# Kernel optimization log

Measured on AMD Instinct MI355X. Metric: run time of the kernel, lower is better.

Reference implementation:

```python
import jax, jax.numpy as jnp
import numpy as np

S, C1, C2, N = 4096, 2048, 2048, 1024


def setup_inputs() -> dict:
    key = jax.random.key(0)
    k1, k2, k3, k4 = jax.random.split(key, 4)
    # child log-likelihoods (samples, child_nodes); modest scale so exp() stays finite,
    # matching the (numerically naive) torch forward which exps without max-subtraction.
    ll1 = jax.random.normal(k1, (S, C1), dtype=jnp.float32)
    ll2 = jax.random.normal(k2, (S, C2), dtype=jnp.float32)
    # log edge weights, one tensor per child layer: (nodes, child_nodes)
    w1 = jax.random.normal(k3, (N, C1), dtype=jnp.float32)
    w2 = jax.random.normal(k4, (N, C2), dtype=jnp.float32)
    return {"ll1": ll1, "ll2": ll2, "w1": w1, "w2": w2}


def reference(ll1, ll2, w1, w2):
    # Per child layer: sum_c exp(ll[s,c] + w[n,c]) == exp(ll) @ exp(w).T  -> (S, N)
    # (same math as unsqueeze/repeat/exp/sum in the torch code, without the (S,C,N) blowup)
    result = jnp.exp(ll1) @ jnp.exp(w1).T + jnp.exp(ll2) @ jnp.exp(w2).T  # (S, N)
    # per-node log normalization constant over concatenated weights
    log_z = jax.nn.logsumexp(jnp.concatenate([w1, w2], axis=1), axis=1)  # (N,)
    return jnp.log(result) - log_z[None, :]
```

## Files before the change

### kernel.cpp

```cpp
#include <hip/hip_runtime.h>

#define S_DIM 4096
#define C_DIM 2048
#define N_DIM 1024
#define K_DIM 4096

#define BM 128
#define BN 128
#define BK 32
#define NT (K_DIM / BK)
#define TILE_BYTES 16384
#define NBUF 8

typedef __attribute__((ext_vector_type(8))) short bf16x8;
typedef __attribute__((ext_vector_type(4))) float f32x4;

__device__ static inline unsigned short f2bf(float f) {
    unsigned int u = __float_as_uint(f);
    u += 0x7FFFu + ((u >> 16) & 1u);
    return (unsigned short)(u >> 16);
}

__global__ void exp_ll_kernel(const float* __restrict__ ll1,
                              const float* __restrict__ ll2,
                              unsigned short* __restrict__ A) {
    const int total4 = S_DIM * C_DIM / 4;
    int stride = gridDim.x * blockDim.x;
    for (int i = blockIdx.x * blockDim.x + threadIdx.x; i < total4; i += stride) {
        int e = i << 2;
        int r = e >> 11;
        int c = e & 2047;
        size_t dst = ((size_t)r << 12) + c;
        float4 v = *reinterpret_cast<const float4*>(ll1 + e);
        ushort4 o;
        o.x = f2bf(__expf(v.x)); o.y = f2bf(__expf(v.y));
        o.z = f2bf(__expf(v.z)); o.w = f2bf(__expf(v.w));
        *reinterpret_cast<ushort4*>(A + dst) = o;
        float4 u = *reinterpret_cast<const float4*>(ll2 + e);
        ushort4 p;
        p.x = f2bf(__expf(u.x)); p.y = f2bf(__expf(u.y));
        p.z = f2bf(__expf(u.z)); p.w = f2bf(__expf(u.w));
        *reinterpret_cast<ushort4*>(A + dst + C_DIM) = p;
    }
}

__global__ void w_kernel(const float* __restrict__ w1,
                         const float* __restrict__ w2,
                         unsigned short* __restrict__ B,
                         float* __restrict__ lz) {
    const int n = blockIdx.x;
    const int tid = threadIdx.x;
    const int lane = tid & 63, wv = tid >> 6;
    const float* r1 = w1 + ((size_t)n << 11);
    const float* r2 = w2 + ((size_t)n << 11);
    float4 v0 = *reinterpret_cast<const float4*>(r1 + tid * 8);
    float4 v1 = *reinterpret_cast<const float4*>(r1 + tid * 8 + 4);
    float4 u0 = *reinterpret_cast<const float4*>(r2 + tid * 8);
    float4 u1 = *reinterpret_cast<const float4*>(r2 + tid * 8 + 4);

    float mx = fmaxf(fmaxf(fmaxf(v0.x, v0.y), fmaxf(v0.z, v0.w)),
                     fmaxf(fmaxf(v1.x, v1.y), fmaxf(v1.z, v1.w)));
    mx = fmaxf(mx, fmaxf(fmaxf(fmaxf(u0.x, u0.y), fmaxf(u0.z, u0.w)),
                          fmaxf(fmaxf(u1.x, u1.y), fmaxf(u1.z, u1.w))));
    #pragma unroll
    for (int off = 32; off > 0; off >>= 1) mx = fmaxf(mx, __shfl_xor(mx, off));
    __shared__ float red[4];
    if (lane == 0) red[wv] = mx;
    __syncthreads();
    mx = fmaxf(fmaxf(red[0], red[1]), fmaxf(red[2], red[3]));

    float s = __expf(v0.x - mx) + __expf(v0.y - mx) + __expf(v0.z - mx) + __expf(v0.w - mx)
            + __expf(v1.x - mx) + __expf(v1.y - mx) + __expf(v1.z - mx) + __expf(v1.w - mx)
            + __expf(u0.x - mx) + __expf(u0.y - mx) + __expf(u0.z - mx) + __expf(u0.w - mx)
            + __expf(u1.x - mx) + __expf(u1.y - mx) + __expf(u1.z - mx) + __expf(u1.w - mx);
    #pragma unroll
    for (int off = 32; off > 0; off >>= 1) s += __shfl_xor(s, off);
    __shared__ float red2[4];
    if (lane == 0) red2[wv] = s;
    __syncthreads();
    if (tid == 0)
        lz[n] = mx + __logf(red2[0] + red2[1] + red2[2] + red2[3]);

    unsigned short* brow = B + ((size_t)n << 12);
    ushort4 o;
    o.x = f2bf(__expf(v0.x)); o.y = f2bf(__expf(v0.y));
    o.z = f2bf(__expf(v0.z)); o.w = f2bf(__expf(v0.w));
    *reinterpret_cast<ushort4*>(brow + tid * 8) = o;
    o.x = f2bf(__expf(v1.x)); o.y = f2bf(__expf(v1.y));
    o.z = f2bf(__expf(v1.z)); o.w = f2bf(__expf(v1.w));
    *reinterpret_cast<ushort4*>(brow + tid * 8 + 4) = o;
    o.x = f2bf(__expf(u0.x)); o.y = f2bf(__expf(u0.y));
    o.z = f2bf(__expf(u0.z)); o.w = f2bf(__expf(u0.w));
    *reinterpret_cast<ushort4*>(brow + C_DIM + tid * 8) = o;
    o.x = f2bf(__expf(u1.x)); o.y = f2bf(__expf(u1.y));
    o.z = f2bf(__expf(u1.z)); o.w = f2bf(__expf(u1.w));
    *reinterpret_cast<ushort4*>(brow + C_DIM + tid * 8 + 4) = o;
}

typedef const unsigned int __attribute__((address_space(1)))* gas_ptr;
typedef unsigned int __attribute__((address_space(3)))* las_ptr;

__global__ __launch_bounds__(512, 2) void gemm_log_kernel(
        const unsigned short* __restrict__ A,
        const unsigned short* __restrict__ B,
        const float* __restrict__ lz,
        float* __restrict__ out) {
    __shared__ __align__(16) char lds[NBUF * TILE_BYTES];
    const int tid  = threadIdx.x;
    const int l    = tid & 63;
    const int w    = tid >> 6;
    const int bn = blockIdx.x & 7;
    const int bm = blockIdx.x >> 3;

#define GLOAD(p_, o_) __builtin_amdgcn_global_load_lds((gas_ptr)(const void*)(p_), \
        (las_ptr)(void*)(lds + (o_)), 16, 0, 0)

    if (w >= 4) {
        const int pw = w - 4;
        const int kg = (l & 3) ^ ((l >> 3) & 3);
        const unsigned short* src[4];
        int dst[4];
        #pragma unroll
        for (int i = 0; i < 4; ++i) {
            const int ri  = pw * 4 + i;
            const int row = ri * 16 + (l >> 2);
            src[i] = (ri < 8)
                ? A + (size_t)(bm * BM + row) * K_DIM + kg * 8
                : B + (size_t)(bn * BN + row - 128) * K_DIM + kg * 8;
            dst[i] = row * 64 + (l & 3) * 16;
        }
#define STAGE(T, BUFI) { const int _ko = (T) * BK; const int _bo = (BUFI) * TILE_BYTES; \
        GLOAD(src[0] + _ko, _bo + dst[0]); GLOAD(src[1] + _ko, _bo + dst[1]);           \
        GLOAD(src[2] + _ko, _bo + dst[2]); GLOAD(src[3] + _ko, _bo + dst[3]); }
#define PBODY(T, BUFI, WAITN) {                                                         \
        asm volatile("s_waitcnt vmcnt(" #WAITN ")" ::: "memory");                       \
        __builtin_amdgcn_s_barrier();                                                   \
        STAGE((T) + 8, BUFI); }

        STAGE(0, 0); STAGE(1, 1); STAGE(2, 2); STAGE(3, 3);
        STAGE(4, 4); STAGE(5, 5); STAGE(6, 6); STAGE(7, 7);
        asm volatile("s_waitcnt vmcnt(28)" ::: "memory");
        __builtin_amdgcn_s_barrier();
        for (int t8 = 0; t8 < NT - 8; t8 += 8) {
            PBODY(t8 + 0, 0, 24); PBODY(t8 + 1, 1, 24);
            PBODY(t8 + 2, 2, 24); PBODY(t8 + 3, 3, 24);
            PBODY(t8 + 4, 4, 24); PBODY(t8 + 5, 5, 24);
            PBODY(t8 + 6, 6, 24); PBODY(t8 + 7, 7, 24);
        }
        asm volatile("s_waitcnt vmcnt(24)" ::: "memory"); __builtin_amdgcn_s_barrier();
        asm volatile("s_waitcnt vmcnt(20)" ::: "memory"); __builtin_amdgcn_s_barrier();
        asm volatile("s_waitcnt vmcnt(16)" ::: "memory"); __builtin_amdgcn_s_barrier();
        asm volatile("s_waitcnt vmcnt(12)" ::: "memory"); __builtin_amdgcn_s_barrier();
        asm volatile("s_waitcnt vmcnt(8)"  ::: "memory"); __builtin_amdgcn_s_barrier();
        asm volatile("s_waitcnt vmcnt(4)"  ::: "memory"); __builtin_amdgcn_s_barrier();
        asm volatile("s_waitcnt vmcnt(0)"  ::: "memory"); __builtin_amdgcn_s_barrier();
#undef PBODY
#undef STAGE
    } else {
        const int wr = w >> 1, wc = w & 1;
        const int lcol = l & 15, lk = l >> 4;
        const int swz = (lk ^ ((lcol >> 1) & 3)) << 4;
        int aoff[4], boff[4];
        #pragma unroll
        for (int m = 0; m < 4; ++m) aoff[m] = (wr * 64 + m * 16 + lcol) * 64 + swz;
        #pragma unroll
        for (int n = 0; n < 4; ++n) boff[n] = 8192 + (wc * 64 + n * 16 + lcol) * 64 + swz;

        f32x4 acc[4][4] = {};
        bf16x8 a0[4], b0[4], a1[4], b1[4];

#define READF(RBUF, AR, BR) { const char* _rb = lds + (RBUF) * TILE_BYTES;              \
        _Pragma("unroll") for (int m = 0; m < 4; ++m)                                   \
            AR[m] = *reinterpret_cast<const bf16x8*>(_rb + aoff[m]);                    \
        _Pragma("unroll") for (int n = 0; n < 4; ++n)                                   \
            BR[n] = *reinterpret_cast<const bf16x8*>(_rb + boff[n]); }
#define MFMAS(AMM, BMM) {                                                               \
        __builtin_amdgcn_s_setprio(1);                                                  \
        _Pragma("unroll") for (int m = 0; m < 4; ++m)                                   \
            _Pragma("unroll") for (int n = 0; n < 4; ++n)                               \
                acc[m][n] = __builtin_amdgcn_mfma_f32_16x16x32_bf16(AMM[m], BMM[n],     \
                                                                    acc[m][n], 0, 0, 0);\
        __builtin_amdgcn_s_setprio(0); }
#define CBODY(T, RB, AR, BR, AMM, BMM) {                                                \
        __builtin_amdgcn_s_barrier();                                                   \
        READF(RB, AR, BR);                                                              \
        MFMAS(AMM, BMM); }

        __builtin_amdgcn_s_barrier();
        READF(0, a0, b0);
        for (int t8 = 0; t8 < NT - 8; t8 += 8) {
            CBODY(t8 + 0, 1, a1, b1, a0, b0);
            CBODY(t8 + 1, 2, a0, b0, a1, b1);
            CBODY(t8 + 2, 3, a1, b1, a0, b0);
            CBODY(t8 + 3, 4, a0, b0, a1, b1);
            CBODY(t8 + 4, 5, a1, b1, a0, b0);
            CBODY(t8 + 5, 6, a0, b0, a1, b1);
            CBODY(t8 + 6, 7, a1, b1, a0, b0);
            CBODY(t8 + 7, 0, a0, b0, a1, b1);
        }
        CBODY(120, 1, a1, b1, a0, b0);
        CBODY(121, 2, a0, b0, a1, b1);
        CBODY(122, 3, a1, b1, a0, b0);
        CBODY(123, 4, a0, b0, a1, b1);
        CBODY(124, 5, a1, b1, a0, b0);
        CBODY(125, 6, a0, b0, a1, b1);
        CBODY(126, 7, a1, b1, a0, b0);
        MFMAS(a1, b1);
#undef CBODY
#undef MFMAS
#undef READF

        const int col_base = bn * BN + wc * 64;
        float lzv[4];
        #pragma unroll
        for (int n = 0; n < 4; ++n) lzv[n] = lz[col_base + n * 16 + lcol];
        #pragma unroll
        for (int m = 0; m < 4; ++m) {
            const int row0 = bm * BM + wr * 64 + m * 16 + lk * 4;
            #pragma unroll
            for (int n = 0; n < 4; ++n) {
                const int col = col_base + n * 16 + lcol;
                #pragma unroll
                for (int j = 0; j < 4; ++j)
                    out[(size_t)(row0 + j) * N_DIM + col] = __logf(acc[m][n][j]) - lzv[n];
            }
        }
    }
#undef GLOAD
}

__global__ void naive_kernel(const float* __restrict__ ll1, const float* __restrict__ ll2,
                             const float* __restrict__ w1, const float* __restrict__ w2,
                             float* __restrict__ out) {
    int idx = blockIdx.x * blockDim.x + threadIdx.x;
    if (idx >= S_DIM * N_DIM) return;
    int s = idx >> 10, n = idx & (N_DIM - 1);
    const float* a1 = ll1 + (size_t)s * C_DIM;
    const float* a2 = ll2 + (size_t)s * C_DIM;
    const float* b1 = w1 + (size_t)n * C_DIM;
    const float* b2 = w2 + (size_t)n * C_DIM;
    float mx = -3.0e38f;
    for (int c = 0; c < C_DIM; ++c) mx = fmaxf(mx, b1[c]);
    for (int c = 0; c < C_DIM; ++c) mx = fmaxf(mx, b2[c]);
    float zs = 0.f, acc = 0.f;
    for (int c = 0; c < C_DIM; ++c) { zs += __expf(b1[c] - mx); acc += __expf(a1[c] + b1[c]); }
    for (int c = 0; c < C_DIM; ++c) { zs += __expf(b2[c] - mx); acc += __expf(a2[c] + b2[c]); }
    out[idx] = __logf(acc) - (mx + __logf(zs));
}

extern "C" void kernel_launch(void* const* d_in, const int* in_sizes, int n_in,
                              void* d_out, int out_size, void* d_ws, size_t ws_size,
                              hipStream_t stream) {
    const float* ll1 = (const float*)d_in[0];
    const float* ll2 = (const float*)d_in[1];
    const float* w1  = (const float*)d_in[2];
    const float* w2  = (const float*)d_in[3];
    float* out = (float*)d_out;

    const size_t a_elems = (size_t)S_DIM * K_DIM;
    const size_t b_elems = (size_t)N_DIM * K_DIM;
    const size_t need = (a_elems + b_elems) * sizeof(unsigned short) + N_DIM * sizeof(float);
    if (ws_size < need) {
        naive_kernel<<<(S_DIM * N_DIM + 255) / 256, 256, 0, stream>>>(ll1, ll2, w1, w2, out);
        return;
    }
    unsigned short* Aws = (unsigned short*)d_ws;
    unsigned short* Bws = Aws + a_elems;
    float* lzws = (float*)(Bws + b_elems);

    exp_ll_kernel<<<2048, 256, 0, stream>>>(ll1, ll2, Aws);
    w_kernel<<<N_DIM, 256, 0, stream>>>(w1, w2, Bws, lzws);
    gemm_log_kernel<<<(S_DIM / BM) * (N_DIM / BN), 512, 0, stream>>>(Aws, Bws, lzws, out);
}
```

Baseline: 70.77 us.

## Reshape GEMM tile to 64x256 with 6-deep LDS ring and XCD-aware block mapping

Changes the block tile from 128x128 to 64x256, so each producer warp now issues five async global-to-LDS loads per stage, and shrinks the ring buffer from 8 to 6 stages of 20 KB. Block indices are remapped so that each group of four XCDs shares the same row band and the B column tiles land on fixed XCDs, aiming for better L2 reuse. Occupancy drops to one block per CU in launch bounds, which trades latency hiding for a wider N tile. Per-block bytes loaded per FLOP rise slightly (64+256 vs 128+128), so the gain depends on the cache-locality improvement.

```diff
diff --git a/kernel.cpp b/kernel.cpp
--- a/kernel.cpp
+++ b/kernel.cpp
@@ -5,12 +5,12 @@
 #define N_DIM 1024
 #define K_DIM 4096
 
-#define BM 128
-#define BN 128
+#define BM 64
+#define BN 256
 #define BK 32
 #define NT (K_DIM / BK)
-#define TILE_BYTES 16384
-#define NBUF 8
+#define TILE_BYTES 20480
+#define NBUF 6
 
 typedef __attribute__((ext_vector_type(8))) short bf16x8;
 typedef __attribute__((ext_vector_type(4))) float f32x4;
@@ -100,7 +100,7 @@
 typedef const unsigned int __attribute__((address_space(1)))* gas_ptr;
 typedef unsigned int __attribute__((address_space(3)))* las_ptr;
 
-__global__ __launch_bounds__(512, 2) void gemm_log_kernel(
+__global__ __launch_bounds__(512, 1) void gemm_log_kernel(
         const unsigned short* __restrict__ A,
         const unsigned short* __restrict__ B,
         const float* __restrict__ lz,
@@ -109,8 +109,10 @@
     const int tid  = threadIdx.x;
     const int l    = tid & 63;
     const int w    = tid >> 6;
-    const int bn = blockIdx.x & 7;
-    const int bm = blockIdx.x >> 3;
+    const int xcd  = blockIdx.x & 7;
+    const int slot = blockIdx.x >> 3;
+    const int bn = xcd & 3;
+    const int bm = slot + ((xcd >> 2) << 5);
 
 #define GLOAD(p_, o_) __builtin_amdgcn_global_load_lds((gas_ptr)(const void*)(p_), \
         (las_ptr)(void*)(lds + (o_)), 16, 0, 0)
@@ -118,53 +120,52 @@
     if (w >= 4) {
         const int pw = w - 4;
         const int kg = (l & 3) ^ ((l >> 3) & 3);
-        const unsigned short* src[4];
-        int dst[4];
-        #pragma unroll
-        for (int i = 0; i < 4; ++i) {
-            const int ri  = pw * 4 + i;
+        const unsigned short* src[5];
+        int dst[5];
+        #pragma unroll
+        for (int i = 0; i < 5; ++i) {
+            const int ri  = pw * 5 + i;
             const int row = ri * 16 + (l >> 2);
-            src[i] = (ri < 8)
+            src[i] = (ri < 4)
                 ? A + (size_t)(bm * BM + row) * K_DIM + kg * 8
-                : B + (size_t)(bn * BN + row - 128) * K_DIM + kg * 8;
+                : B + (size_t)(bn * BN + row - 64) * K_DIM + kg * 8;
             dst[i] = row * 64 + (l & 3) * 16;
         }
 #define STAGE(T, BUFI) { const int _ko = (T) * BK; const int _bo = (BUFI) * TILE_BYTES; \
         GLOAD(src[0] + _ko, _bo + dst[0]); GLOAD(src[1] + _ko, _bo + dst[1]);           \
-        GLOAD(src[2] + _ko, _bo + dst[2]); GLOAD(src[3] + _ko, _bo + dst[3]); }
-#define PBODY(T, BUFI, WAITN) {                                                         \
-        asm volatile("s_waitcnt vmcnt(" #WAITN ")" ::: "memory");                       \
+        GLOAD(src[2] + _ko, _bo + dst[2]); GLOAD(src[3] + _ko, _bo + dst[3]);           \
+        GLOAD(src[4] + _ko, _bo + dst[4]); }
+#define PBODY(T, BUFI) {                                                                \
+        asm volatile("s_waitcnt vmcnt(20)" ::: "memory");                               \
         __builtin_amdgcn_s_barrier();                                                   \
-        STAGE((T) + 8, BUFI); }
-
-        STAGE(0, 0); STAGE(1, 1); STAGE(2, 2); STAGE(3, 3);
-        STAGE(4, 4); STAGE(5, 5); STAGE(6, 6); STAGE(7, 7);
-        asm volatile("s_waitcnt vmcnt(28)" ::: "memory");
+        STAGE((T) + 6, BUFI); }
+
+        STAGE(0, 0); STAGE(1, 1); STAGE(2, 2);
+        STAGE(3, 3); STAGE(4, 4); STAGE(5, 5);
+        asm volatile("s_waitcnt vmcnt(25)" ::: "memory");
         __builtin_amdgcn_s_barrier();
-        for (int t8 = 0; t8 < NT - 8; t8 += 8) {
-            PBODY(t8 + 0, 0, 24); PBODY(t8 + 1, 1, 24);
-            PBODY(t8 + 2, 2, 24); PBODY(t8 + 3, 3, 24);
-            PBODY(t8 + 4, 4, 24); PBODY(t8 + 5, 5, 24);
-            PBODY(t8 + 6, 6, 24); PBODY(t8 + 7, 7, 24);
-        }
-        asm volatile("s_waitcnt vmcnt(24)" ::: "memory"); __builtin_amdgcn_s_barrier();
+        for (int t6 = 0; t6 < NT - 14; t6 += 6) {
+            PBODY(t6 + 0, 0); PBODY(t6 + 1, 1); PBODY(t6 + 2, 2);
+            PBODY(t6 + 3, 3); PBODY(t6 + 4, 4); PBODY(t6 + 5, 5);
+        }
+        PBODY(114, 0); PBODY(115, 1); PBODY(116, 2);
+        PBODY(117, 3); PBODY(118, 4); PBODY(119, 5);
+        PBODY(120, 0); PBODY(121, 1);
         asm volatile("s_waitcnt vmcnt(20)" ::: "memory"); __builtin_amdgcn_s_barrier();
-        asm volatile("s_waitcnt vmcnt(16)" ::: "memory"); __builtin_amdgcn_s_barrier();
-        asm volatile("s_waitcnt vmcnt(12)" ::: "memory"); __builtin_amdgcn_s_barrier();
-        asm volatile("s_waitcnt vmcnt(8)"  ::: "memory"); __builtin_amdgcn_s_barrier();
-        asm volatile("s_waitcnt vmcnt(4)"  ::: "memory"); __builtin_amdgcn_s_barrier();
+        asm volatile("s_waitcnt vmcnt(15)" ::: "memory"); __builtin_amdgcn_s_barrier();
+        asm volatile("s_waitcnt vmcnt(10)" ::: "memory"); __builtin_amdgcn_s_barrier();
+        asm volatile("s_waitcnt vmcnt(5)"  ::: "memory"); __builtin_amdgcn_s_barrier();
         asm volatile("s_waitcnt vmcnt(0)"  ::: "memory"); __builtin_amdgcn_s_barrier();
 #undef PBODY
 #undef STAGE
     } else {
-        const int wr = w >> 1, wc = w & 1;
         const int lcol = l & 15, lk = l >> 4;
         const int swz = (lk ^ ((lcol >> 1) & 3)) << 4;
         int aoff[4], boff[4];
         #pragma unroll
-        for (int m = 0; m < 4; ++m) aoff[m] = (wr * 64 + m * 16 + lcol) * 64 + swz;
-        #pragma unroll
-        for (int n = 0; n < 4; ++n) boff[n] = 8192 + (wc * 64 + n * 16 + lcol) * 64 + swz;
+        for (int m = 0; m < 4; ++m) aoff[m] = (m * 16 + lcol) * 64 + swz;
+        #pragma unroll
+        for (int n = 0; n < 4; ++n) boff[n] = 4096 + (w * 64 + n * 16 + lcol) * 64 + swz;
 
         f32x4 acc[4][4] = {};
         bf16x8 a0[4], b0[4], a1[4], b1[4];
@@ -181,42 +182,43 @@
                 acc[m][n] = __builtin_amdgcn_mfma_f32_16x16x32_bf16(AMM[m], BMM[n],     \
                                                                     acc[m][n], 0, 0, 0);\
         __builtin_amdgcn_s_setprio(0); }
-#define CBODY(T, RB, AR, BR, AMM, BMM) {                                                \
+#define CBODY(RB, AR, BR, AMM, BMM) {                                                   \
         __builtin_amdgcn_s_barrier();                                                   \
         READF(RB, AR, BR);                                                              \
         MFMAS(AMM, BMM); }
 
         __builtin_amdgcn_s_barrier();
         READF(0, a0, b0);
-        for (int t8 = 0; t8 < NT - 8; t8 += 8) {
-            CBODY(t8 + 0, 1, a1, b1, a0, b0);
-            CBODY(t8 + 1, 2, a0, b0, a1, b1);
-            CBODY(t8 + 2, 3, a1, b1, a0, b0);
-            CBODY(t8 + 3, 4, a0, b0, a1, b1);
-            CBODY(t8 + 4, 5, a1, b1, a0, b0);
-            CBODY(t8 + 5, 6, a0, b0, a1, b1);
-            CBODY(t8 + 6, 7, a1, b1, a0, b0);
-            CBODY(t8 + 7, 0, a0, b0, a1, b1);
-        }
-        CBODY(120, 1, a1, b1, a0, b0);
-        CBODY(121, 2, a0, b0, a1, b1);
-        CBODY(122, 3, a1, b1, a0, b0);
-        CBODY(123, 4, a0, b0, a1, b1);
-        CBODY(124, 5, a1, b1, a0, b0);
-        CBODY(125, 6, a0, b0, a1, b1);
-        CBODY(126, 7, a1, b1, a0, b0);
+        for (int t6 = 0; t6 < NT - 14; t6 += 6) {
+            CBODY(1, a1, b1, a0, b0); CBODY(2, a0, b0, a1, b1);
+            CBODY(3, a1, b1, a0, b0); CBODY(4, a0, b0, a1, b1);
+            CBODY(5, a1, b1, a0, b0); CBODY(0, a0, b0, a1, b1);
+        }
+        CBODY(1, a1, b1, a0, b0);
+        CBODY(2, a0, b0, a1, b1);
+        CBODY(3, a1, b1, a0, b0);
+        CBODY(4, a0, b0, a1, b1);
+        CBODY(5, a1, b1, a0, b0);
+        CBODY(0, a0, b0, a1, b1);
+        CBODY(1, a1, b1, a0, b0);
+        CBODY(2, a0, b0, a1, b1);
+        CBODY(3, a1, b1, a0, b0);
+        CBODY(4, a0, b0, a1, b1);
+        CBODY(5, a1, b1, a0, b0);
+        CBODY(0, a0, b0, a1, b1);
+        CBODY(1, a1, b1, a0, b0);
         MFMAS(a1, b1);
 #undef CBODY
 #undef MFMAS
 #undef READF
 
-        const int col_base = bn * BN + wc * 64;
+        const int col_base = bn * BN + w * 64;
         float lzv[4];
         #pragma unroll
         for (int n = 0; n < 4; ++n) lzv[n] = lz[col_base + n * 16 + lcol];
         #pragma unroll
         for (int m = 0; m < 4; ++m) {
-            const int row0 = bm * BM + wr * 64 + m * 16 + lk * 4;
+            const int row0 = bm * BM + m * 16 + lk * 4;
             #pragma unroll
             for (int n = 0; n < 4; ++n) {
                 const int col = col_base + n * 16 + lcol;
```

After: 78.06 us. 10.3% more time.
